# Kernel tuning notes

Hardware: AMD Instinct MI355X
Metric: run time of the kernel (lower is better)

Reference implementation:

```python
import jax, jax.numpy as jnp
import numpy as np

IN_DIMS = 512
TOKEN_DIM = 512
NUM_HEADS = 1
D = TOKEN_DIM * NUM_HEADS
SCALE = TOKEN_DIM ** (-0.5)
EPS = 1e-12  # torch F.normalize default


def _l2norm(v, axis):
    n = jnp.sqrt(jnp.sum(v * v, axis=axis, keepdims=True))
    return v / jnp.maximum(n, EPS)


def setup_inputs() -> dict:
    key = jax.random.key(0)
    ks = jax.random.split(key, 10)
    B, C, H, W = 64, IN_DIMS, 28, 28
    s_in = IN_DIMS ** -0.5
    s_d = D ** -0.5
    return {
        "x": jax.random.normal(ks[0], (B, C, H, W), jnp.float32),
        "Wq": jax.random.normal(ks[1], (IN_DIMS, D), jnp.float32) * s_in,
        "bq": jax.random.normal(ks[2], (D,), jnp.float32) * 0.01,
        "Wk": jax.random.normal(ks[3], (IN_DIMS, D), jnp.float32) * s_in,
        "bk": jax.random.normal(ks[4], (D,), jnp.float32) * 0.01,
        "w_g": jax.random.normal(ks[5], (D, 1), jnp.float32),
        "Wp": jax.random.normal(ks[6], (D, D), jnp.float32) * s_d,
        "bp": jax.random.normal(ks[7], (D,), jnp.float32) * 0.01,
        "Wf": jax.random.normal(ks[8], (D, TOKEN_DIM), jnp.float32) * s_d,
        "bf": jax.random.normal(ks[9], (TOKEN_DIM,), jnp.float32) * 0.01,
    }


def reference(x, Wq, bq, Wk, bk, w_g, Wp, bp, Wf, bf):
    B, C, H, W = x.shape
    t = x.reshape(B, C, H * W).transpose(0, 2, 1)          # [B, N, C]
    query = _l2norm(t @ Wq + bq, axis=-1)                  # [B, N, D]
    k = _l2norm(t @ Wk + bk, axis=-1)                      # [B, N, D]
    attn = _l2norm((query @ w_g) * SCALE, axis=1)          # [B, N, 1], normalized over tokens
    ctx = jnp.sum(attn * query, axis=1, keepdims=True)     # [B, 1, D] global context
    out = (ctx * k) @ Wp + bp + query                      # [B, N, D]
    out = out @ Wf + bf                                    # [B, N, TOKEN_DIM]
    return out.transpose(0, 2, 1).reshape(B, -1, H, W)
```

## Files before the change

kernel.cpp:

```cpp
#include <hip/hip_runtime.h>

#define EPSN 1e-12f
#define SCALE_F 0.044194173824159216f
#define MTOT 50176

typedef __bf16 bf16x8 __attribute__((ext_vector_type(8)));
typedef float  f32x4  __attribute__((ext_vector_type(4)));

__device__ __forceinline__ void gld16(const void* src, void* dst) {
  __builtin_amdgcn_global_load_lds(
      (const __attribute__((address_space(1))) unsigned int*)src,
      (__attribute__((address_space(3))) unsigned int*)dst, 16, 0, 0);
}

__global__ __launch_bounds__(256) void k_xt(const float* __restrict__ x,
                                            __bf16* __restrict__ xT, int b0) {
  __shared__ float T[32][33];
  const int n0 = blockIdx.x * 32, c0 = blockIdx.y * 32;
  const int bl = blockIdx.z, b = b0 + bl;
  const int dx = threadIdx.x, ty = threadIdx.y;
  #pragma unroll
  for (int pp = 0; pp < 4; ++pp) {
    int c = ty + pp * 8;
    int n = n0 + dx;
    T[c][dx] = (n < 784) ? x[((size_t)b * 512 + c0 + c) * 784 + n] : 0.f;
  }
  __syncthreads();
  #pragma unroll
  for (int pp = 0; pp < 4; ++pp) {
    int n = ty + pp * 8;
    if (n0 + n < 784)
      xT[((size_t)bl * 784 + n0 + n) * 512 + c0 + dx] = (__bf16)T[dx][n];
  }
}

__global__ __launch_bounds__(256) void k_prep_t(const float* __restrict__ Wq,
                                                const float* __restrict__ Wk,
                                                __bf16* __restrict__ WqT,
                                                __bf16* __restrict__ WkT) {
  __shared__ float Tq[32][33], Tk[32][33];
  const int c0 = blockIdx.x * 32, d0 = blockIdx.y * 32;
  const int dx = threadIdx.x, cy = threadIdx.y;
  #pragma unroll
  for (int p = 0; p < 4; ++p) {
    int c = cy + p * 8;
    Tq[c][dx] = Wq[(size_t)(c0 + c) * 512 + d0 + dx];
    Tk[c][dx] = Wk[(size_t)(c0 + c) * 512 + d0 + dx];
  }
  __syncthreads();
  #pragma unroll
  for (int p = 0; p < 4; ++p) {
    int d = cy + p * 8;
    WqT[(size_t)(d0 + d) * 512 + c0 + dx] = (__bf16)Tq[dx][d];
    WkT[(size_t)(d0 + d) * 512 + c0 + dx] = (__bf16)Tk[dx][d];
  }
}

__global__ __launch_bounds__(512) void k_prep_w(const float* __restrict__ Wp,
                                                const float* __restrict__ Wf,
                                                const float* __restrict__ bp,
                                                const float* __restrict__ bfv,
                                                __bf16* __restrict__ WcT,
                                                float* __restrict__ bpf) {
  const int kk0 = blockIdx.x * 2;
  const int d = threadIdx.x;
  float acc0 = 0.f, acc1 = 0.f, bacc = 0.f;
  const bool dobp = (blockIdx.x == 0);
  for (int c = 0; c < 512; ++c) {
    float wf = Wf[(size_t)c * 512 + d];
    acc0 = fmaf(Wp[(size_t)kk0 * 512 + c],       wf, acc0);
    acc1 = fmaf(Wp[(size_t)(kk0 + 1) * 512 + c], wf, acc1);
    if (dobp) bacc = fmaf(bp[c], wf, bacc);
  }
  WcT[(size_t)d * 1024 + kk0]           = (__bf16)acc0;
  WcT[(size_t)d * 1024 + kk0 + 1]       = (__bf16)acc1;
  WcT[(size_t)d * 1024 + 512 + kk0]     = (__bf16)Wf[(size_t)kk0 * 512 + d];
  WcT[(size_t)d * 1024 + 512 + kk0 + 1] = (__bf16)Wf[(size_t)(kk0 + 1) * 512 + d];
  if (dobp) bpf[d] = bacc + bfv[d];
}

__global__ __launch_bounds__(256, 2) void k_gemm(const __bf16* __restrict__ xT,
                                                 const __bf16* __restrict__ WqT,
                                                 const __bf16* __restrict__ WkT,
                                                 const float* __restrict__ bq,
                                                 const float* __restrict__ bk,
                                                 const float* __restrict__ wg,
                                                 const int b0,
                                                 __bf16* __restrict__ qraw,
                                                 __bf16* __restrict__ kraw,
                                                 float* __restrict__ psqQ,
                                                 float* __restrict__ psqK,
                                                 float* __restrict__ gdo) {
  __shared__ __align__(1024) unsigned char stg[2][24576];
  const int t = threadIdx.x, l = t & 63, w = t >> 6;
  const int li = l & 15, lq = l >> 4;
  const int p = blockIdx.x;
  const int xq = p & 7, q2 = p >> 3;
  const int nt = q2 & 3;
  const int g = (q2 >> 2) * 8 + xq;
  const int bl = g / 7, mt = g % 7;
  const int b = b0 + bl;
  const int m0 = mt * 128;

  const int r0 = 2 * w, r1 = r0 + 1;
  int row0 = m0 + r0 * 16 + li; if (row0 > 783) row0 = 783;
  int row1 = m0 + r1 * 16 + li; if (row1 > 783) row1 = 783;
  const __bf16* a0s = xT + ((size_t)bl * 784 + row0) * 512 + lq * 8;
  const __bf16* a1s = xT + ((size_t)bl * 784 + row1) * 512 + lq * 8;
  const __bf16* q0s = WqT + (size_t)(nt * 128 + r0 * 16 + li) * 512 + lq * 8;
  const __bf16* q1s = WqT + (size_t)(nt * 128 + r1 * 16 + li) * 512 + lq * 8;
  const __bf16* k0s = WkT + (size_t)(nt * 128 + r0 * 16 + li) * 512 + lq * 8;
  const __bf16* k1s = WkT + (size_t)(nt * 128 + r1 * 16 + li) * 512 + lq * 8;

  f32x4 accQ[4][4] = {}, accK[4][4] = {};

  auto stage = [&](int buf, int ks) {
    const int kk = (ks > 15 ? 15 : ks) * 32;
    gld16(a0s + kk, stg[buf] + r0 * 1024);
    gld16(a1s + kk, stg[buf] + r1 * 1024);
    gld16(q0s + kk, stg[buf] + 8192 + r0 * 1024);
    gld16(q1s + kk, stg[buf] + 8192 + r1 * 1024);
    gld16(k0s + kk, stg[buf] + 16384 + r0 * 1024);
    gld16(k1s + kk, stg[buf] + 16384 + r1 * 1024);
  };
  auto mstep = [&](int buf) {
    bf16x8 af[4];
    #pragma unroll
    for (int rb = 0; rb < 4; ++rb)
      af[rb] = *(const bf16x8*)(stg[buf] + ((w & 1) * 4 + rb) * 1024 + l * 16);
    #pragma unroll
    for (int cb = 0; cb < 4; ++cb) {
      bf16x8 bq8 = *(const bf16x8*)(stg[buf] + 8192 + ((w >> 1) * 4 + cb) * 1024 + l * 16);
      #pragma unroll
      for (int rb = 0; rb < 4; ++rb)
        accQ[rb][cb] = __builtin_amdgcn_mfma_f32_16x16x32_bf16(af[rb], bq8, accQ[rb][cb], 0, 0, 0);
      bf16x8 bk8 = *(const bf16x8*)(stg[buf] + 16384 + ((w >> 1) * 4 + cb) * 1024 + l * 16);
      #pragma unroll
      for (int rb = 0; rb < 4; ++rb)
        accK[rb][cb] = __builtin_amdgcn_mfma_f32_16x16x32_bf16(af[rb], bk8, accK[rb][cb], 0, 0, 0);
    }
  };

  stage(0, 0);
  asm volatile("s_waitcnt vmcnt(0)" ::: "memory");
  __builtin_amdgcn_s_barrier();
  __builtin_amdgcn_sched_barrier(0);
  #pragma unroll 1
  for (int ks = 0; ks < 16; ++ks) {
    stage((ks + 1) & 1, ks + 1);
    __builtin_amdgcn_sched_barrier(0);
    mstep(ks & 1);
    asm volatile("s_waitcnt vmcnt(0)" ::: "memory");
    __builtin_amdgcn_s_barrier();
    __builtin_amdgcn_sched_barrier(0);
  }

  const int colb = nt * 128 + (w >> 1) * 64;
  const int cg = nt * 2 + (w >> 1);
  float bqv[4], bkv[4], wv[4];
  #pragma unroll
  for (int cb = 0; cb < 4; ++cb) {
    int col = colb + cb * 16 + li;
    bqv[cb] = bq[col]; bkv[cb] = bk[col]; wv[cb] = wg[col];
  }
  #pragma unroll
  for (int rb = 0; rb < 4; ++rb)
    #pragma unroll
    for (int j = 0; j < 4; ++j) {
      int rowg = m0 + (w & 1) * 64 + rb * 16 + lq * 4 + j;
      bool ok = rowg < 784;
      size_t token = (size_t)b * 784 + rowg;
      float ssq = 0.f, ssk = 0.f, sg = 0.f;
      #pragma unroll
      for (int cb = 0; cb < 4; ++cb) {
        float vq = accQ[rb][cb][j] + bqv[cb];
        float vk = accK[rb][cb][j] + bkv[cb];
        ssq = fmaf(vq, vq, ssq);
        ssk = fmaf(vk, vk, ssk);
        sg  = fmaf(vq, wv[cb], sg);
        if (ok) {
          qraw[token * 512 + colb + cb * 16 + li] = (__bf16)vq;
          kraw[token * 512 + colb + cb * 16 + li] = (__bf16)vk;
        }
      }
      ssq += __shfl_xor(ssq, 1); ssq += __shfl_xor(ssq, 2); ssq += __shfl_xor(ssq, 4); ssq += __shfl_xor(ssq, 8);
      ssk += __shfl_xor(ssk, 1); ssk += __shfl_xor(ssk, 2); ssk += __shfl_xor(ssk, 4); ssk += __shfl_xor(ssk, 8);
      sg  += __shfl_xor(sg, 1);  sg  += __shfl_xor(sg, 2);  sg  += __shfl_xor(sg, 4);  sg  += __shfl_xor(sg, 8);
      if (ok && li == 0) {
        psqQ[(size_t)cg * MTOT + token] = ssq;
        psqK[(size_t)cg * MTOT + token] = ssk;
        gdo [(size_t)cg * MTOT + token] = sg;
      }
    }
}

__global__ __launch_bounds__(256) void k_normc(const float* __restrict__ psqQ,
                                               const float* __restrict__ psqK,
                                               const float* __restrict__ gdo,
                                               float* __restrict__ invqA,
                                               float* __restrict__ invkA,
                                               float* __restrict__ coefA,
                                               float* __restrict__ gA) {
  const int tkn = blockIdx.x * 256 + threadIdx.x;
  if (tkn >= MTOT) return;
  float sq = 0.f, sk = 0.f, gd = 0.f;
  #pragma unroll
  for (int cg = 0; cg < 8; ++cg) {
    sq += psqQ[(size_t)cg * MTOT + tkn];
    sk += psqK[(size_t)cg * MTOT + tkn];
    gd += gdo[(size_t)cg * MTOT + tkn];
  }
  float invq = 1.f / fmaxf(sqrtf(sq), EPSN);
  float invk = 1.f / fmaxf(sqrtf(sk), EPSN);
  float gv = gd * invq;
  invqA[tkn] = invq;
  invkA[tkn] = invk;
  coefA[tkn] = gv * invq;
  gA[tkn]    = gv;
}

__global__ __launch_bounds__(512) void k_pctx(const __bf16* __restrict__ qraw,
                                              const float* __restrict__ coefA,
                                              const float* __restrict__ gA,
                                              float* __restrict__ ctx) {
  __shared__ float wred[8];
  __shared__ float part[4][128];
  const int ch = blockIdx.x, b = blockIdx.y, t = threadIdx.x;
  const size_t base = (size_t)b * 784;
  float gsq;
  { float gv = gA[base + t]; gsq = gv * gv; }
  if (t + 512 < 784) { float gv = gA[base + t + 512]; gsq = fmaf(gv, gv, gsq); }
  gsq += __shfl_xor(gsq, 1);  gsq += __shfl_xor(gsq, 2);  gsq += __shfl_xor(gsq, 4);
  gsq += __shfl_xor(gsq, 8);  gsq += __shfl_xor(gsq, 16); gsq += __shfl_xor(gsq, 32);
  if ((t & 63) == 0) wred[t >> 6] = gsq;
  __syncthreads();
  float tot = 0.f;
  #pragma unroll
  for (int i = 0; i < 8; ++i) tot += wred[i];
  const float alpha = SCALE_F / fmaxf(sqrtf(tot) * SCALE_F, EPSN);
  const int dof = t & 127, s = t >> 7;
  const int nb = s * 196;
  const __bf16* qb = qraw + (base + nb) * 512 + ch * 128 + dof;
  const float* cf = coefA + base + nb;
  float a0 = 0.f, a1 = 0.f, a2 = 0.f, a3 = 0.f;
  for (int n = 0; n < 196; n += 4) {
    a0 = fmaf(cf[n],     (float)qb[(size_t)n * 512],       a0);
    a1 = fmaf(cf[n + 1], (float)qb[(size_t)(n + 1) * 512], a1);
    a2 = fmaf(cf[n + 2], (float)qb[(size_t)(n + 2) * 512], a2);
    a3 = fmaf(cf[n + 3], (float)qb[(size_t)(n + 3) * 512], a3);
  }
  part[s][dof] = (a0 + a1) + (a2 + a3);
  __syncthreads();
  if (t < 128) {
    float sum = part[0][t] + part[1][t] + part[2][t] + part[3][t];
    ctx[(size_t)b * 512 + ch * 128 + t] = alpha * sum;
  }
}

__global__ __launch_bounds__(256, 3) void k_out(const __bf16* __restrict__ qraw,
                                                const __bf16* __restrict__ kraw,
                                                const float* __restrict__ invqA,
                                                const float* __restrict__ invkA,
                                                const float* __restrict__ ctx,
                                                const __bf16* __restrict__ WcT,
                                                const float* __restrict__ bpf,
                                                float* __restrict__ out) {
  __shared__ __align__(1024) unsigned char stg[2][16384];
  __shared__ float ctx_l[512];
  const int t = threadIdx.x, l = t & 63, w = t >> 6;
  const int li = l & 15, lq = l >> 4;
  const int p = blockIdx.x;
  const int xq = p & 7, q2 = p >> 3;
  const int nt = q2 & 3;
  const int g = (q2 >> 2) * 8 + xq;
  const int b = g / 7, mt = g % 7;
  const int m0 = mt * 128;

  ctx_l[t]       = ctx[(size_t)b * 512 + t];
  ctx_l[t + 256] = ctx[(size_t)b * 512 + t + 256];
  __syncthreads();

  const int rA0 = w, rA1 = w + 4;
  int row0 = m0 + rA0 * 16 + li; if (row0 > 783) row0 = 783;
  int row1 = m0 + rA1 * 16 + li; if (row1 > 783) row1 = 783;
  const size_t tk0 = (size_t)b * 784 + row0, tk1 = (size_t)b * 784 + row1;
  const float iq0 = invqA[tk0], ik0 = invkA[tk0];
  const float iq1 = invqA[tk1], ik1 = invkA[tk1];
  const __bf16* wpB0 = WcT + (size_t)(nt * 128 + (2 * w) * 16 + li) * 1024 + lq * 8;
  const __bf16* wpB1 = WcT + (size_t)(nt * 128 + (2 * w + 1) * 16 + li) * 1024 + lq * 8;

  f32x4 acc[4][4] = {};

  auto stageB = [&](int buf, int ks) {
    const int kk = (ks > 31 ? 31 : ks) * 32;
    gld16(wpB0 + kk, stg[buf] + 8192 + (2 * w) * 1024);
    gld16(wpB1 + kk, stg[buf] + 8192 + (2 * w + 1) * 1024);
  };
  auto loadA = [&](bf16x8& v0, bf16x8& v1, int ks) {
    const int kk = ks > 31 ? 31 : ks;
    const __bf16* ap = (kk < 16) ? kraw : qraw;
    const int off = (kk & 15) * 32 + lq * 8;
    v0 = *(const bf16x8*)(ap + tk0 * 512 + off);
    v1 = *(const bf16x8*)(ap + tk1 * 512 + off);
  };
  auto writeA = [&](int buf, bf16x8 v0, bf16x8 v1, int ks) {
    const int kk = ks > 31 ? 31 : ks;
    bf16x8 o0, o1;
    if (kk < 16) {
      const int kl = (kk & 15) * 32 + lq * 8;
      f32x4 c0 = *(const f32x4*)&ctx_l[kl];
      f32x4 c1 = *(const f32x4*)&ctx_l[kl + 4];
      #pragma unroll
      for (int j = 0; j < 4; ++j) {
        o0[j]     = (__bf16)((float)v0[j]     * ik0 * c0[j]);
        o0[4 + j] = (__bf16)((float)v0[4 + j] * ik0 * c1[j]);
        o1[j]     = (__bf16)((float)v1[j]     * ik1 * c0[j]);
        o1[4 + j] = (__bf16)((float)v1[4 + j] * ik1 * c1[j]);
      }
    } else {
      #pragma unroll
      for (int j = 0; j < 8; ++j) {
        o0[j] = (__bf16)((float)v0[j] * iq0);
        o1[j] = (__bf16)((float)v1[j] * iq1);
      }
    }
    *(bf16x8*)(stg[buf] + rA0 * 1024 + l * 16) = o0;
    *(bf16x8*)(stg[buf] + rA1 * 1024 + l * 16) = o1;
  };
  auto mstep = [&](int buf) {
    bf16x8 af[4];
    #pragma unroll
    for (int rb = 0; rb < 4; ++rb)
      af[rb] = *(const bf16x8*)(stg[buf] + ((w & 1) * 4 + rb) * 1024 + l * 16);
    #pragma unroll
    for (int cb = 0; cb < 4; ++cb) {
      bf16x8 bf = *(const bf16x8*)(stg[buf] + 8192 + ((w >> 1) * 4 + cb) * 1024 + l * 16);
      #pragma unroll
      for (int rb = 0; rb < 4; ++rb)
        acc[rb][cb] = __builtin_amdgcn_mfma_f32_16x16x32_bf16(af[rb], bf, acc[rb][cb], 0, 0, 0);
    }
  };

  {
    bf16x8 vA0, vA1;
    loadA(vA0, vA1, 0);
    stageB(0, 0);
    asm volatile("s_waitcnt vmcnt(0)" ::: "memory");
    writeA(0, vA0, vA1, 0);
    asm volatile("s_waitcnt lgkmcnt(0)" ::: "memory");
    __builtin_amdgcn_s_barrier();
    __builtin_amdgcn_sched_barrier(0);
  }
  #pragma unroll 1
  for (int ks = 0; ks < 32; ++ks) {
    bf16x8 nA0, nA1;
    loadA(nA0, nA1, ks + 1);
    stageB((ks + 1) & 1, ks + 1);
    __builtin_amdgcn_sched_barrier(0);
    mstep(ks & 1);
    asm volatile("s_waitcnt vmcnt(0)" ::: "memory");
    writeA((ks + 1) & 1, nA0, nA1, ks + 1);
    asm volatile("s_waitcnt lgkmcnt(0)" ::: "memory");
    __builtin_amdgcn_s_barrier();
    __builtin_amdgcn_sched_barrier(0);
  }

  const int colb = nt * 128 + (w >> 1) * 64;
  float bv[4];
  #pragma unroll
  for (int cb = 0; cb < 4; ++cb) bv[cb] = bpf[colb + cb * 16 + li];
  #pragma unroll
  for (int rb = 0; rb < 4; ++rb) {
    int nrow = m0 + (w & 1) * 64 + rb * 16 + lq * 4;
    if (nrow < 784) {
      #pragma unroll
      for (int cb = 0; cb < 4; ++cb) {
        f32x4 v;
        #pragma unroll
        for (int j = 0; j < 4; ++j) v[j] = acc[rb][cb][j] + bv[cb];
        *(f32x4*)&out[((size_t)b * 512 + colb + cb * 16 + li) * 784 + nrow] = v;
      }
    }
  }
}

extern "C" void kernel_launch(void* const* d_in, const int* in_sizes, int n_in,
                              void* d_out, int out_size, void* d_ws, size_t ws_size,
                              hipStream_t stream) {
  const float* x   = (const float*)d_in[0];
  const float* Wq  = (const float*)d_in[1];
  const float* bq  = (const float*)d_in[2];
  const float* Wk  = (const float*)d_in[3];
  const float* bk  = (const float*)d_in[4];
  const float* wg  = (const float*)d_in[5];
  const float* Wp  = (const float*)d_in[6];
  const float* bp  = (const float*)d_in[7];
  const float* Wf  = (const float*)d_in[8];
  const float* bfv = (const float*)d_in[9];
  float* out = (float*)d_out;
  char* ws = (char*)d_ws;

  const size_t SZRAW = (size_t)MTOT * 512 * 2;
  const size_t SZXT  = (size_t)32 * 784 * 512 * 2;
  size_t off = 0;
  __bf16* qraw = (__bf16*)(ws + off); off += SZRAW;
  __bf16* kraw = (__bf16*)(ws + off); off += SZRAW;
  __bf16* xT   = (__bf16*)(ws + off); off += SZXT;
  __bf16* WqT  = (__bf16*)(ws + off); off += 524288;
  __bf16* WkT  = (__bf16*)(ws + off); off += 524288;
  __bf16* WcT  = (__bf16*)(ws + off); off += 1048576;
  float*  bpf  = (float*) (ws + off); off += 2048;
  float*  psqQ = (float*) (ws + off); off += (size_t)8 * MTOT * 4;
  float*  psqK = (float*) (ws + off); off += (size_t)8 * MTOT * 4;
  float*  gdo  = (float*) (ws + off); off += (size_t)8 * MTOT * 4;
  float*  invqA = (float*)(ws + off); off += (size_t)MTOT * 4;
  float*  invkA = (float*)(ws + off); off += (size_t)MTOT * 4;
  float*  coefA = (float*)(ws + off); off += (size_t)MTOT * 4;
  float*  gA    = (float*)(ws + off); off += (size_t)MTOT * 4;
  float*  ctx   = (float*)(ws + off); off += 131072;

  k_prep_t<<<dim3(16, 16), dim3(32, 8), 0, stream>>>(Wq, Wk, WqT, WkT);
  k_prep_w<<<dim3(256),    dim3(512),   0, stream>>>(Wp, Wf, bp, bfv, WcT, bpf);
  for (int s = 0; s < 2; ++s) {
    k_xt  <<<dim3(25, 16, 32), dim3(32, 8), 0, stream>>>(x, xT, s * 32);
    k_gemm<<<dim3(896),        dim3(256),   0, stream>>>(xT, WqT, WkT, bq, bk, wg, s * 32,
                                                         qraw, kraw, psqQ, psqK, gdo);
  }
  k_normc<<<dim3(196),   dim3(256), 0, stream>>>(psqQ, psqK, gdo, invqA, invkA, coefA, gA);
  k_pctx <<<dim3(4, 64), dim3(512), 0, stream>>>(qraw, coefA, gA, ctx);
  k_out  <<<dim3(1792),  dim3(256), 0, stream>>>(qraw, kraw, invqA, invkA, ctx, WcT, bpf, out);
}
```

Baseline: 402.4 us.

## Triple-buffer LDS staging in QK and output GEMMs for deeper prefetch

Both main GEMM kernels go from double-buffered to triple-buffered LDS staging. Loads are issued two k-steps ahead, and the waits become partial vmcnt counts instead of full drains, so global loads overlap more with MFMA work. The output kernel's loop is unrolled by two so the register-held A fragments can alternate through the three buffers. LDS per block grows by half, which may lower occupancy (the QK kernel goes to 72KB per block at 2 blocks per CU), and correctness now depends on the vmcnt counts matching the number of loads in flight.

```diff
diff --git a/kernel.cpp b/kernel.cpp
--- a/kernel.cpp
+++ b/kernel.cpp
@@ -91,7 +91,7 @@
                                                  float* __restrict__ psqQ,
                                                  float* __restrict__ psqK,
                                                  float* __restrict__ gdo) {
-  __shared__ __align__(1024) unsigned char stg[2][24576];
+  __shared__ __align__(1024) unsigned char stg[3][24576];
   const int t = threadIdx.x, l = t & 63, w = t >> 6;
   const int li = l & 15, lq = l >> 4;
   const int p = blockIdx.x;
@@ -114,46 +114,49 @@
 
   f32x4 accQ[4][4] = {}, accK[4][4] = {};
 
-  auto stage = [&](int buf, int ks) {
+  auto stage = [&](unsigned char* buf, int ks) {
     const int kk = (ks > 15 ? 15 : ks) * 32;
-    gld16(a0s + kk, stg[buf] + r0 * 1024);
-    gld16(a1s + kk, stg[buf] + r1 * 1024);
-    gld16(q0s + kk, stg[buf] + 8192 + r0 * 1024);
-    gld16(q1s + kk, stg[buf] + 8192 + r1 * 1024);
-    gld16(k0s + kk, stg[buf] + 16384 + r0 * 1024);
-    gld16(k1s + kk, stg[buf] + 16384 + r1 * 1024);
-  };
-  auto mstep = [&](int buf) {
+    gld16(a0s + kk, buf + r0 * 1024);
+    gld16(a1s + kk, buf + r1 * 1024);
+    gld16(q0s + kk, buf + 8192 + r0 * 1024);
+    gld16(q1s + kk, buf + 8192 + r1 * 1024);
+    gld16(k0s + kk, buf + 16384 + r0 * 1024);
+    gld16(k1s + kk, buf + 16384 + r1 * 1024);
+  };
+  auto mstep = [&](const unsigned char* buf) {
     bf16x8 af[4];
     #pragma unroll
     for (int rb = 0; rb < 4; ++rb)
-      af[rb] = *(const bf16x8*)(stg[buf] + ((w & 1) * 4 + rb) * 1024 + l * 16);
+      af[rb] = *(const bf16x8*)(buf + ((w & 1) * 4 + rb) * 1024 + l * 16);
     #pragma unroll
     for (int cb = 0; cb < 4; ++cb) {
-      bf16x8 bq8 = *(const bf16x8*)(stg[buf] + 8192 + ((w >> 1) * 4 + cb) * 1024 + l * 16);
+      bf16x8 bq8 = *(const bf16x8*)(buf + 8192 + ((w >> 1) * 4 + cb) * 1024 + l * 16);
       #pragma unroll
       for (int rb = 0; rb < 4; ++rb)
         accQ[rb][cb] = __builtin_amdgcn_mfma_f32_16x16x32_bf16(af[rb], bq8, accQ[rb][cb], 0, 0, 0);
-      bf16x8 bk8 = *(const bf16x8*)(stg[buf] + 16384 + ((w >> 1) * 4 + cb) * 1024 + l * 16);
+      bf16x8 bk8 = *(const bf16x8*)(buf + 16384 + ((w >> 1) * 4 + cb) * 1024 + l * 16);
       #pragma unroll
       for (int rb = 0; rb < 4; ++rb)
         accK[rb][cb] = __builtin_amdgcn_mfma_f32_16x16x32_bf16(af[rb], bk8, accK[rb][cb], 0, 0, 0);
     }
   };
 
-  stage(0, 0);
-  asm volatile("s_waitcnt vmcnt(0)" ::: "memory");
+  unsigned char *bc = stg[0], *bn = stg[1], *bn2 = stg[2];
+  stage(bc, 0); stage(bn, 1);
+  asm volatile("s_waitcnt vmcnt(6)" ::: "memory");
   __builtin_amdgcn_s_barrier();
   __builtin_amdgcn_sched_barrier(0);
   #pragma unroll 1
   for (int ks = 0; ks < 16; ++ks) {
-    stage((ks + 1) & 1, ks + 1);
-    __builtin_amdgcn_sched_barrier(0);
-    mstep(ks & 1);
-    asm volatile("s_waitcnt vmcnt(0)" ::: "memory");
+    stage(bn2, ks + 2);
+    __builtin_amdgcn_sched_barrier(0);
+    mstep(bc);
+    asm volatile("s_waitcnt vmcnt(6)" ::: "memory");
     __builtin_amdgcn_s_barrier();
     __builtin_amdgcn_sched_barrier(0);
-  }
+    unsigned char* tmp = bc; bc = bn; bn = bn2; bn2 = tmp;
+  }
+  asm volatile("s_waitcnt vmcnt(0)" ::: "memory");
 
   const int colb = nt * 128 + (w >> 1) * 64;
   const int cg = nt * 2 + (w >> 1);
@@ -265,7 +268,7 @@
                                                 const __bf16* __restrict__ WcT,
                                                 const float* __restrict__ bpf,
                                                 float* __restrict__ out) {
-  __shared__ __align__(1024) unsigned char stg[2][16384];
+  __shared__ __align__(1024) unsigned char stg[3][16384];
   __shared__ float ctx_l[512];
   const int t = threadIdx.x, l = t & 63, w = t >> 6;
   const int li = l & 15, lq = l >> 4;
@@ -291,10 +294,10 @@
 
   f32x4 acc[4][4] = {};
 
-  auto stageB = [&](int buf, int ks) {
+  auto stageB = [&](unsigned char* buf, int ks) {
     const int kk = (ks > 31 ? 31 : ks) * 32;
-    gld16(wpB0 + kk, stg[buf] + 8192 + (2 * w) * 1024);
-    gld16(wpB1 + kk, stg[buf] + 8192 + (2 * w + 1) * 1024);
+    gld16(wpB0 + kk, buf + 8192 + (2 * w) * 1024);
+    gld16(wpB1 + kk, buf + 8192 + (2 * w + 1) * 1024);
   };
   auto loadA = [&](bf16x8& v0, bf16x8& v1, int ks) {
     const int kk = ks > 31 ? 31 : ks;
@@ -303,7 +306,7 @@
     v0 = *(const bf16x8*)(ap + tk0 * 512 + off);
     v1 = *(const bf16x8*)(ap + tk1 * 512 + off);
   };
-  auto writeA = [&](int buf, bf16x8 v0, bf16x8 v1, int ks) {
+  auto writeA = [&](unsigned char* buf, bf16x8 v0, bf16x8 v1, int ks) {
     const int kk = ks > 31 ? 31 : ks;
     bf16x8 o0, o1;
     if (kk < 16) {
@@ -324,46 +327,61 @@
         o1[j] = (__bf16)((float)v1[j] * iq1);
       }
     }
-    *(bf16x8*)(stg[buf] + rA0 * 1024 + l * 16) = o0;
-    *(bf16x8*)(stg[buf] + rA1 * 1024 + l * 16) = o1;
-  };
-  auto mstep = [&](int buf) {
+    *(bf16x8*)(buf + rA0 * 1024 + l * 16) = o0;
+    *(bf16x8*)(buf + rA1 * 1024 + l * 16) = o1;
+  };
+  auto mstep = [&](const unsigned char* buf) {
     bf16x8 af[4];
     #pragma unroll
     for (int rb = 0; rb < 4; ++rb)
-      af[rb] = *(const bf16x8*)(stg[buf] + ((w & 1) * 4 + rb) * 1024 + l * 16);
+      af[rb] = *(const bf16x8*)(buf + ((w & 1) * 4 + rb) * 1024 + l * 16);
     #pragma unroll
     for (int cb = 0; cb < 4; ++cb) {
-      bf16x8 bf = *(const bf16x8*)(stg[buf] + 8192 + ((w >> 1) * 4 + cb) * 1024 + l * 16);
+      bf16x8 bf = *(const bf16x8*)(buf + 8192 + ((w >> 1) * 4 + cb) * 1024 + l * 16);
       #pragma unroll
       for (int rb = 0; rb < 4; ++rb)
         acc[rb][cb] = __builtin_amdgcn_mfma_f32_16x16x32_bf16(af[rb], bf, acc[rb][cb], 0, 0, 0);
     }
   };
 
-  {
-    bf16x8 vA0, vA1;
-    loadA(vA0, vA1, 0);
-    stageB(0, 0);
-    asm volatile("s_waitcnt vmcnt(0)" ::: "memory");
-    writeA(0, vA0, vA1, 0);
+  unsigned char *bc = stg[0], *bn = stg[1], *bn2 = stg[2];
+  bf16x8 aA0, aA1, aB0, aB1;
+  loadA(aA0, aA1, 0);
+  stageB(bc, 0);
+  loadA(aB0, aB1, 1);
+  stageB(bn, 1);
+  asm volatile("s_waitcnt vmcnt(4)" ::: "memory");
+  __builtin_amdgcn_sched_barrier(0);
+  writeA(bc, aA0, aA1, 0);
+  asm volatile("s_waitcnt lgkmcnt(0)" ::: "memory");
+  __builtin_amdgcn_s_barrier();
+  __builtin_amdgcn_sched_barrier(0);
+
+  #pragma unroll 1
+  for (int ks = 0; ks < 32; ks += 2) {
+    loadA(aA0, aA1, ks + 2);
+    stageB(bn2, ks + 2);
+    __builtin_amdgcn_sched_barrier(0);
+    mstep(bc);
+    asm volatile("s_waitcnt vmcnt(4)" ::: "memory");
+    __builtin_amdgcn_sched_barrier(0);
+    writeA(bn, aB0, aB1, ks + 1);
     asm volatile("s_waitcnt lgkmcnt(0)" ::: "memory");
     __builtin_amdgcn_s_barrier();
     __builtin_amdgcn_sched_barrier(0);
-  }
-  #pragma unroll 1
-  for (int ks = 0; ks < 32; ++ks) {
-    bf16x8 nA0, nA1;
-    loadA(nA0, nA1, ks + 1);
-    stageB((ks + 1) & 1, ks + 1);
-    __builtin_amdgcn_sched_barrier(0);
-    mstep(ks & 1);
-    asm volatile("s_waitcnt vmcnt(0)" ::: "memory");
-    writeA((ks + 1) & 1, nA0, nA1, ks + 1);
+    loadA(aB0, aB1, ks + 3);
+    stageB(bc, ks + 3);
+    __builtin_amdgcn_sched_barrier(0);
+    mstep(bn);
+    asm volatile("s_waitcnt vmcnt(4)" ::: "memory");
+    __builtin_amdgcn_sched_barrier(0);
+    writeA(bn2, aA0, aA1, ks + 2);
     asm volatile("s_waitcnt lgkmcnt(0)" ::: "memory");
     __builtin_amdgcn_s_barrier();
     __builtin_amdgcn_sched_barrier(0);
-  }
+    unsigned char* tmp = bc; bc = bn2; bn2 = bn; bn = tmp;
+  }
+  asm volatile("s_waitcnt vmcnt(0)" ::: "memory");
 
   const int colb = nt * 128 + (w >> 1) * 64;
   float bv[4];
```

Result: no change. 402.5 us (+0.0%).
